# Kernel optimization log

Hardware: AMD Instinct MI355X
Metric: run time of the kernel (lower is better)

The kernel has to match this reference:

```python
import math
import jax, jax.numpy as jnp
import numpy as np


def bernstein_basis(s, k):
    # s: [N] in [0,1]; returns [N, k] with B_i(s) = C(k-1,i) s^i (1-s)^(k-1-i)
    l = k - 1
    i = jnp.arange(k, dtype=s.dtype)
    comb = jnp.asarray([math.comb(l, ii) for ii in range(k)], dtype=s.dtype)
    return comb * s[:, None] ** i * (1.0 - s[:, None]) ** (l - i)


def setup_inputs() -> dict:
    key = jax.random.key(0)
    k1, k2 = jax.random.split(key)
    N, kx, ky, kz = 1000000, 6, 6, 6
    vertices = jax.random.uniform(k1, (N, 3), dtype=jnp.float32) * 2.0 - 1.0  # in [-1,1]
    p = jax.random.uniform(k2, (3, kx, ky, kz), dtype=jnp.float32)
    return {"vertices": vertices, "p": p}


def reference(vertices, p):
    # vertices: [N,3] in [-1,1]; p: [3,kx,ky,kz]
    kx, ky, kz = p.shape[1], p.shape[2], p.shape[3]
    tar = (vertices + 1.0) * 0.5  # normalize_zero_to_one, [N,3]
    Bx = bernstein_basis(tar[:, 0], kx)  # [N,kx]
    By = bernstein_basis(tar[:, 1], ky)  # [N,ky]
    Bz = bernstein_basis(tar[:, 2], kz)  # [N,kz]
    # staged contraction replacing the kx*ky*kz loop of elementwise kernels
    t1 = jnp.einsum('nk,cijk->ncij', Bz, p)   # [N,3,kx,ky]
    t2 = jnp.einsum('nj,ncij->nci', By, t1)   # [N,3,kx]
    q = jnp.einsum('ni,nci->nc', Bx, t2)      # [N,3]
    q = 2.0 * q - 1.0  # normalize_minus_one_to_one
    return q[None, :, :]  # [1,N,3], matching q.permute(0,2,1)
```

## Files before the change

kernel.cpp:

```cpp
#include <hip/hip_runtime.h>

__device__ __constant__ float Mb[6][6] = {
    { 0.03125f, -0.15625f,  0.3125f, -0.3125f,  0.15625f, -0.03125f},
    { 0.15625f, -0.46875f,  0.3125f,  0.3125f, -0.46875f,  0.15625f},
    { 0.3125f,  -0.3125f,  -0.625f,   0.625f,   0.3125f,  -0.3125f },
    { 0.3125f,   0.3125f,  -0.625f,  -0.625f,   0.3125f,   0.3125f },
    { 0.15625f,  0.46875f,  0.3125f, -0.3125f, -0.46875f, -0.15625f},
    { 0.03125f,  0.15625f,  0.3125f,  0.3125f,  0.15625f,  0.03125f},
};

__global__ __launch_bounds__(256) void ffd_coeffs(const float* __restrict__ p,
                                                  float* __restrict__ A)
{
    __shared__ float b0[648];
    __shared__ float b1[648];
    const int t = threadIdx.x;

    for (int m = t; m < 648; m += 256) b0[m] = p[m];
    __syncthreads();

    for (int m = t; m < 648; m += 256) {
        const int dk = m % 6;
        const int base = (m / 6) * 6;
        float s = 0.f;
        #pragma unroll
        for (int k = 0; k < 6; ++k) s = fmaf(b0[base + k], Mb[k][dk], s);
        b1[m] = s;
    }
    __syncthreads();

    for (int m = t; m < 648; m += 256) {
        const int dk = m % 6;
        const int dj = (m / 6) % 6;
        const int ci = m / 36;
        float s = 0.f;
        #pragma unroll
        for (int j = 0; j < 6; ++j) s = fmaf(b1[(ci * 6 + j) * 6 + dk], Mb[j][dj], s);
        b0[m] = s;
    }
    __syncthreads();

    for (int m = t; m < 648; m += 256) {
        const int dk = m % 6;
        const int dj = (m / 6) % 6;
        const int di = (m / 36) % 6;
        const int c  = m / 216;
        float s = 0.f;
        #pragma unroll
        for (int i = 0; i < 6; ++i) s = fmaf(b0[((c * 6 + i) * 6 + dj) * 6 + dk], Mb[i][di], s);
        s *= 2.0f;
        if (di == 0 && dj == 0 && dk == 0) s -= 1.0f;
        A[m] = s;
    }
}

__global__ __launch_bounds__(256) void ffd_eval(const float* __restrict__ verts,
                                                const float* __restrict__ A,
                                                float* __restrict__ out, int N)
{
    const long long v0 = ((long long)blockIdx.x * 256 + threadIdx.x) * 2;
    if (v0 >= N) return;

    float x[2], y[2], z[2];
    const bool full = (v0 + 2 <= N);
    if (full) {
        const float2* vp = (const float2*)(verts + v0 * 3);
        const float2 f0 = vp[0], f1 = vp[1], f2 = vp[2];
        x[0] = f0.x; y[0] = f0.y; z[0] = f1.x;
        x[1] = f1.y; y[1] = f2.x; z[1] = f2.y;
    } else {
        for (int v = 0; v < 2; ++v) {
            long long n = v0 + v; if (n >= N) n = N - 1;
            x[v] = verts[n * 3 + 0]; y[v] = verts[n * 3 + 1]; z[v] = verts[n * 3 + 2];
        }
    }

    float res[6];
    #pragma unroll
    for (int c = 0; c < 3; ++c) {
        float q0 = 0.f, q1 = 0.f;
        #pragma unroll 1
        for (int ii = 0; ii < 6; ++ii) {
            const int i = 5 - ii;
            const int off = __builtin_amdgcn_readfirstlane((c * 6 + i) * 36);
            const float* __restrict__ Ab = A + off;
            float a[36];
            #pragma unroll
            for (int r = 0; r < 36; ++r) a[r] = Ab[r];

            float t0 = 0.f, t1 = 0.f;
            #pragma unroll
            for (int jj = 0; jj < 6; ++jj) {
                const int j = 5 - jj;
                const float* Ak = a + j * 6;
                float s0 = fmaf(Ak[5], z[0], Ak[4]);
                s0 = fmaf(s0, z[0], Ak[3]);
                s0 = fmaf(s0, z[0], Ak[2]);
                s0 = fmaf(s0, z[0], Ak[1]);
                s0 = fmaf(s0, z[0], Ak[0]);
                float s1 = fmaf(Ak[5], z[1], Ak[4]);
                s1 = fmaf(s1, z[1], Ak[3]);
                s1 = fmaf(s1, z[1], Ak[2]);
                s1 = fmaf(s1, z[1], Ak[1]);
                s1 = fmaf(s1, z[1], Ak[0]);
                t0 = (jj == 0) ? s0 : fmaf(t0, y[0], s0);
                t1 = (jj == 0) ? s1 : fmaf(t1, y[1], s1);
            }
            q0 = (ii == 0) ? t0 : fmaf(q0, x[0], t0);
            q1 = (ii == 0) ? t1 : fmaf(q1, x[1], t1);
        }
        res[c]     = q0;
        res[3 + c] = q1;
    }

    if (full) {
        float2* op = (float2*)(out + v0 * 3);
        op[0] = make_float2(res[0], res[1]);
        op[1] = make_float2(res[2], res[3]);
        op[2] = make_float2(res[4], res[5]);
    } else {
        for (int v = 0; v < 2; ++v) {
            const long long n = v0 + v;
            if (n < N) {
                out[n * 3 + 0] = res[v * 3 + 0];
                out[n * 3 + 1] = res[v * 3 + 1];
                out[n * 3 + 2] = res[v * 3 + 2];
            }
        }
    }
}

extern "C" void kernel_launch(void* const* d_in, const int* in_sizes, int n_in,
                              void* d_out, int out_size, void* d_ws, size_t ws_size,
                              hipStream_t stream)
{
    const float* verts = (const float*)d_in[0];
    const float* p     = (const float*)d_in[1];
    float* out = (float*)d_out;
    float* A   = (float*)d_ws;
    const int N = in_sizes[0] / 3;

    ffd_coeffs<<<1, 256, 0, stream>>>(p, A);

    const int nthreads = (N + 1) / 2;
    const int blocks = (nthreads + 255) / 256;
    ffd_eval<<<blocks, 256, 0, stream>>>(verts, A, out, N);
}
```

Baseline: 80.71 us.

## Fuse coefficient transform into eval kernel, computing per block in LDS

Drops the single-block coefficient kernel and has every eval block recompute the 648 power-basis coefficients into shared memory before evaluating its vertices. The eval loop now reads coefficients from LDS with float4 loads instead of scalar global loads, and the i loop is fully unrolled. This removes one kernel launch and the serial dependency on a one-block kernel. In exchange, each of roughly two thousand blocks repeats the small transform behind three barriers, and the full unroll raises register pressure.

```diff
diff --git a/kernel.cpp b/kernel.cpp
--- a/kernel.cpp
+++ b/kernel.cpp
@@ -9,11 +9,12 @@
     { 0.03125f,  0.15625f,  0.3125f,  0.3125f,  0.15625f,  0.03125f},
 };
 
-__global__ __launch_bounds__(256) void ffd_coeffs(const float* __restrict__ p,
-                                                  float* __restrict__ A)
+__global__ __launch_bounds__(256) void ffd_fused(const float* __restrict__ verts,
+                                                 const float* __restrict__ p,
+                                                 float* __restrict__ out, int N)
 {
-    __shared__ float b0[648];
-    __shared__ float b1[648];
+    __shared__ __align__(16) float b0[648];
+    __shared__ __align__(16) float b1[648];
     const int t = threadIdx.x;
 
     for (int m = t; m < 648; m += 256) b0[m] = p[m];
@@ -50,15 +51,11 @@
         for (int i = 0; i < 6; ++i) s = fmaf(b0[((c * 6 + i) * 6 + dj) * 6 + dk], Mb[i][di], s);
         s *= 2.0f;
         if (di == 0 && dj == 0 && dk == 0) s -= 1.0f;
-        A[m] = s;
+        b1[m] = s;
     }
-}
+    __syncthreads();
 
-__global__ __launch_bounds__(256) void ffd_eval(const float* __restrict__ verts,
-                                                const float* __restrict__ A,
-                                                float* __restrict__ out, int N)
-{
-    const long long v0 = ((long long)blockIdx.x * 256 + threadIdx.x) * 2;
+    const long long v0 = ((long long)blockIdx.x * 256 + t) * 2;
     if (v0 >= N) return;
 
     float x[2], y[2], z[2];
@@ -79,15 +76,17 @@
     #pragma unroll
     for (int c = 0; c < 3; ++c) {
         float q0 = 0.f, q1 = 0.f;
-        #pragma unroll 1
+        #pragma unroll
         for (int ii = 0; ii < 6; ++ii) {
             const int i = 5 - ii;
-            const int off = __builtin_amdgcn_readfirstlane((c * 6 + i) * 36);
-            const float* __restrict__ Ab = A + off;
+            const float4* blk = (const float4*)(b1 + (c * 6 + i) * 36);
             float a[36];
             #pragma unroll
-            for (int r = 0; r < 36; ++r) a[r] = Ab[r];
-
+            for (int r = 0; r < 9; ++r) {
+                const float4 f = blk[r];
+                a[r * 4 + 0] = f.x; a[r * 4 + 1] = f.y;
+                a[r * 4 + 2] = f.z; a[r * 4 + 3] = f.w;
+            }
             float t0 = 0.f, t1 = 0.f;
             #pragma unroll
             for (int jj = 0; jj < 6; ++jj) {
@@ -137,12 +136,9 @@
     const float* verts = (const float*)d_in[0];
     const float* p     = (const float*)d_in[1];
     float* out = (float*)d_out;
-    float* A   = (float*)d_ws;
     const int N = in_sizes[0] / 3;
-
-    ffd_coeffs<<<1, 256, 0, stream>>>(p, A);
 
     const int nthreads = (N + 1) / 2;
     const int blocks = (nthreads + 255) / 256;
-    ffd_eval<<<blocks, 256, 0, stream>>>(verts, A, out, N);
+    ffd_fused<<<blocks, 256, 0, stream>>>(verts, p, out, N);
 }
```

Result: slower. 95.00 us (+17.7%).
